# Kernel tuning notes

Hardware: AMD Instinct MI355X
Metric: run time of the kernel (lower is better)

## Reference

```python
import jax, jax.numpy as jnp
import numpy as np

B, T, I, H = 256, 512, 128, 256


def setup_inputs() -> dict:
    key = jax.random.key(0)
    ks = jax.random.split(key, 12)
    xav = lambda k, shape: jax.random.normal(k, shape, jnp.float32) * jnp.sqrt(2.0 / (shape[0] + shape[1]))
    return {
        'x': jax.random.normal(ks[0], (B, T, I), jnp.float32),
        'weight_xr': xav(ks[1], (H, I)), 'weight_hr': xav(ks[2], (H, H)), 'bias_r': jnp.zeros((H,), jnp.float32),
        'weight_xz': xav(ks[3], (H, I)), 'weight_hz': xav(ks[4], (H, H)), 'bias_z': jnp.zeros((H,), jnp.float32),
        'weight_x': xav(ks[5], (H, I)), 'weight_h': xav(ks[6], (H, H)), 'bias': jnp.zeros((H,), jnp.float32),
        'w1': xav(ks[7], (64, H)), 'b1': jnp.zeros((64,), jnp.float32),
        'w2': xav(ks[8], (10, 64)), 'b2': jnp.zeros((10,), jnp.float32),
    }


def _gru_final(x, weight_xr, weight_hr, bias_r, weight_xz, weight_hz, bias_z,
               weight_x, weight_h, bias):
    # Precompute input projections for all timesteps: [B,T,H] each
    xr = jnp.einsum('bti,hi->bth', x, weight_xr) + bias_r
    xz = jnp.einsum('bti,hi->bth', x, weight_xz) + bias_z
    xn = jnp.einsum('bti,hi->bth', x, weight_x) + bias

    def step(h, inp):
        xr_t, xz_t, xn_t = inp  # each [B,H]
        r = jax.nn.sigmoid(xr_t + h @ weight_hr.T)
        z = jax.nn.sigmoid(xz_t + h @ weight_hz.T)
        ht = jnp.tanh(xn_t + (r * h) @ weight_h.T)
        h_new = z * h + (1.0 - z) * ht
        return h_new, None

    h0 = jnp.zeros((x.shape[0], weight_hr.shape[0]), x.dtype)
    # scan over time: inputs [T,B,H]
    h_final, _ = jax.lax.scan(step, h0, (xr.transpose(1, 0, 2), xz.transpose(1, 0, 2), xn.transpose(1, 0, 2)))
    return h_final


def reference(x, weight_xr, weight_hr, bias_r, weight_xz, weight_hz, bias_z,
              weight_x, weight_h, bias, w1, b1, w2, b2):
    h = _gru_final(x, weight_xr, weight_hr, bias_r, weight_xz, weight_hz, bias_z,
                   weight_x, weight_h, bias)
    h = jax.nn.sigmoid(h)
    h = jax.nn.sigmoid(h @ w1.T + b1)
    return jax.nn.softmax(h @ w2.T + b2, axis=1)
```

## Files before the change

kernel.cpp:

```cpp
#include <hip/hip_runtime.h>


typedef _Float16 half8 __attribute__((ext_vector_type(8)));
typedef float    f32x4 __attribute__((ext_vector_type(4)));

#define BARRIER() asm volatile("s_waitcnt lgkmcnt(0)\n\ts_barrier" ::: "memory")

__device__ __forceinline__ unsigned short f2s(float f) {
    _Float16 h = (_Float16)f; unsigned short s; __builtin_memcpy(&s, &h, 2); return s;
}
__device__ __forceinline__ float s2f(unsigned short s) {
    _Float16 h; __builtin_memcpy(&h, &s, 2); return (float)h;
}
__device__ __forceinline__ float fast_sigmoid(float x) {
    return __builtin_amdgcn_rcpf(1.0f + __builtin_amdgcn_exp2f(-1.4426950408889634f * x));
}
__device__ __forceinline__ float fast_tanh(float x) {
    return 1.0f - 2.0f * __builtin_amdgcn_rcpf(1.0f + __builtin_amdgcn_exp2f(2.885390081777927f * x));
}
__device__ __forceinline__ unsigned int pk2(float lo, float hi) {
    return (unsigned int)f2s(lo) | ((unsigned int)f2s(hi) << 16);
}
union H8U4 { half8 h; uint4 u; };
__device__ __forceinline__ half8 ldg_h8(const unsigned short* p) {
    H8U4 t; t.u = *reinterpret_cast<const uint4*>(p); return t.h;
}
__device__ __forceinline__ half8 pack8(float4 a, float4 b) {
    half8 r;
    r[0] = (_Float16)a.x; r[1] = (_Float16)a.y; r[2] = (_Float16)a.z; r[3] = (_Float16)a.w;
    r[4] = (_Float16)b.x; r[5] = (_Float16)b.y; r[6] = (_Float16)b.z; r[7] = (_Float16)b.w;
    return r;
}

__global__ void pack_w_kernel(const float* __restrict__ whr, const float* __restrict__ whz,
                              const float* __restrict__ wh,  const float* __restrict__ wxr,
                              const float* __restrict__ wxz, const float* __restrict__ wxn,
                              unsigned short* __restrict__ Wall) {
    const int i = blockIdx.x * 256 + threadIdx.x;
    float v;
    if (i < 196608) {
        const int m = i >> 16;
        const int r = i & 65535;
        v = (m == 0 ? whr : (m == 1 ? whz : wh))[r];
    } else {
        const int ii = i - 196608;
        const int m = ii >> 15;
        const int r = ii & 32767;
        v = (m == 0 ? wxr : (m == 1 ? wxz : wxn))[r];
    }
    Wall[i] = f2s(v);
}

__global__ __launch_bounds__(256) void proj_kernel(
    const float* __restrict__ x, const unsigned short* __restrict__ Wxp,
    const float* __restrict__ br, const float* __restrict__ bz, const float* __restrict__ bn,
    unsigned short* __restrict__ P, int t0) {
    const int tid = threadIdx.x;
    const int wv  = tid >> 6;
    const int lane = tid & 63;
    const int l15 = lane & 15;
    const int lq  = lane >> 4;
    const int tl = blockIdx.x >> 4;
    const int btile = blockIdx.x & 15;
    const int t = t0 + tl;
    const int b0 = btile * 16;

    half8 xf[4];
#pragma unroll
    for (int kt = 0; kt < 4; ++kt) {
        const float* xp = x + (size_t)(b0 + l15) * 65536 + t * 128 + kt * 32 + 8 * lq;
        float4 f0 = *reinterpret_cast<const float4*>(xp);
        float4 f1 = *reinterpret_cast<const float4*>(xp + 4);
        xf[kt] = pack8(f0, f1);
    }
    const float* bptr[3] = {br, bz, bn};
    unsigned short* Pb = P + (size_t)tl * 196608 + btile * 12288;
#pragma unroll
    for (int g = 0; g < 3; ++g) {
#pragma unroll
        for (int ntl = 0; ntl < 4; ++ntl) {
            const int nt = wv * 4 + ntl;
            const int n0 = nt * 16;
            f32x4 acc = {0.f, 0.f, 0.f, 0.f};
#pragma unroll
            for (int kt = 0; kt < 4; ++kt) {
                half8 wf = ldg_h8(Wxp + g * 32768 + (n0 + l15) * 128 + kt * 32 + 8 * lq);
                acc = __builtin_amdgcn_mfma_f32_16x16x32_f16(wf, xf[kt], acc, 0, 0, 0);
            }
            float4 bv = *reinterpret_cast<const float4*>(bptr[g] + n0 + 4 * lq);
            uint2 o;
            o.x = pk2(acc[0] + bv.x, acc[1] + bv.y);
            o.y = pk2(acc[2] + bv.z, acc[3] + bv.w);
            *reinterpret_cast<uint2*>(Pb + nt * 768 + g * 256 + lane * 4) = o;
        }
    }
}

__global__ __launch_bounds__(512, 1) void rec_kernel(
    const unsigned short* __restrict__ Wp, const unsigned short* __restrict__ P,
    float* __restrict__ h_state, int t0, int Tc) {
    const int tid = threadIdx.x;
    const int w = tid >> 6;
    const int lane = tid & 63;
    const int l15 = lane & 15;
    const int lq = lane >> 4;
    const int btile = blockIdx.x;
    const int b0 = btile * 16;

    __shared__ __align__(16) unsigned short hl[8192];

    half8 wr[8][2], wz[8][2], wn[8][2];
#pragma unroll
    for (int kt = 0; kt < 8; ++kt) {
#pragma unroll
        for (int nt = 0; nt < 2; ++nt) {
            const int row = w * 32 + nt * 16 + l15;
            const int co = kt * 32 + 8 * lq;
            wr[kt][nt] = ldg_h8(Wp + row * 256 + co);
            wz[kt][nt] = ldg_h8(Wp + 65536 + row * 256 + co);
            wn[kt][nt] = ldg_h8(Wp + 131072 + row * 256 + co);
        }
    }

    const int b7 = l15 & 7;
    int rdaddr[8];
#pragma unroll
    for (int kt = 0; kt < 8; ++kt)
        rdaddr[kt] = l15 * 512 + (((4 * kt + lq) ^ b7) << 4);
    int waddr[2];
#pragma unroll
    for (int nt = 0; nt < 2; ++nt) {
        const int c = 4 * w + 2 * nt + (lq >> 1);
        waddr[nt] = l15 * 512 + ((c ^ b7) << 4) + 8 * (lq & 1);
    }

    float hreg[2][4];
    if (t0 == 0) {
#pragma unroll
        for (int nt = 0; nt < 2; ++nt)
#pragma unroll
            for (int j = 0; j < 4; ++j) hreg[nt][j] = 0.f;
    } else {
#pragma unroll
        for (int nt = 0; nt < 2; ++nt) {
            float4 v = *reinterpret_cast<const float4*>(
                h_state + (b0 + l15) * 256 + w * 32 + nt * 16 + 4 * lq);
            hreg[nt][0] = v.x; hreg[nt][1] = v.y; hreg[nt][2] = v.z; hreg[nt][3] = v.w;
        }
    }
#pragma unroll
    for (int nt = 0; nt < 2; ++nt) {
        uint2 o;
        o.x = pk2(hreg[nt][0], hreg[nt][1]);
        o.y = pk2(hreg[nt][2], hreg[nt][3]);
        *reinterpret_cast<uint2*>(reinterpret_cast<char*>(hl) + waddr[nt]) = o;
    }
    BARRIER();

    const unsigned short* Pw = P + btile * 12288 + (2 * w) * 768 + lane * 4;
    uint2 cp[3][2], np[3][2];
#pragma unroll
    for (int g = 0; g < 3; ++g)
#pragma unroll
        for (int nt = 0; nt < 2; ++nt)
            cp[g][nt] = *reinterpret_cast<const uint2*>(Pw + nt * 768 + g * 256);

    for (int tl = 0; tl < Tc; ++tl) {
        const unsigned short* Pn = Pw + (size_t)((tl + 1 < Tc) ? tl + 1 : tl) * 196608;
#pragma unroll
        for (int g = 0; g < 3; ++g)
#pragma unroll
            for (int nt = 0; nt < 2; ++nt)
                np[g][nt] = *reinterpret_cast<const uint2*>(Pn + nt * 768 + g * 256);

        f32x4 aR[2], aZ[2];
#pragma unroll
        for (int nt = 0; nt < 2; ++nt) {
            aR[nt] = (f32x4){ s2f((unsigned short)cp[0][nt].x), s2f((unsigned short)(cp[0][nt].x >> 16)),
                              s2f((unsigned short)cp[0][nt].y), s2f((unsigned short)(cp[0][nt].y >> 16)) };
            aZ[nt] = (f32x4){ s2f((unsigned short)cp[1][nt].x), s2f((unsigned short)(cp[1][nt].x >> 16)),
                              s2f((unsigned short)cp[1][nt].y), s2f((unsigned short)(cp[1][nt].y >> 16)) };
        }
#pragma unroll
        for (int kt = 0; kt < 8; ++kt) {
            half8 hf = *reinterpret_cast<const half8*>(reinterpret_cast<const char*>(hl) + rdaddr[kt]);
            aR[0] = __builtin_amdgcn_mfma_f32_16x16x32_f16(wr[kt][0], hf, aR[0], 0, 0, 0);
            aZ[0] = __builtin_amdgcn_mfma_f32_16x16x32_f16(wz[kt][0], hf, aZ[0], 0, 0, 0);
            aR[1] = __builtin_amdgcn_mfma_f32_16x16x32_f16(wr[kt][1], hf, aR[1], 0, 0, 0);
            aZ[1] = __builtin_amdgcn_mfma_f32_16x16x32_f16(wz[kt][1], hf, aZ[1], 0, 0, 0);
        }
        float zv[2][4];
#pragma unroll
        for (int nt = 0; nt < 2; ++nt) {
            float r0 = fast_sigmoid(aR[nt][0]);
            float r1 = fast_sigmoid(aR[nt][1]);
            float r2 = fast_sigmoid(aR[nt][2]);
            float r3 = fast_sigmoid(aR[nt][3]);
            zv[nt][0] = fast_sigmoid(aZ[nt][0]);
            zv[nt][1] = fast_sigmoid(aZ[nt][1]);
            zv[nt][2] = fast_sigmoid(aZ[nt][2]);
            zv[nt][3] = fast_sigmoid(aZ[nt][3]);
            uint2 o;
            o.x = pk2(r0 * hreg[nt][0], r1 * hreg[nt][1]);
            o.y = pk2(r2 * hreg[nt][2], r3 * hreg[nt][3]);
            *reinterpret_cast<uint2*>(reinterpret_cast<char*>(hl) + 8192 + waddr[nt]) = o;
        }
        BARRIER();

        f32x4 aN[2];
#pragma unroll
        for (int nt = 0; nt < 2; ++nt) {
            aN[nt] = (f32x4){ s2f((unsigned short)cp[2][nt].x), s2f((unsigned short)(cp[2][nt].x >> 16)),
                              s2f((unsigned short)cp[2][nt].y), s2f((unsigned short)(cp[2][nt].y >> 16)) };
        }
#pragma unroll
        for (int kt = 0; kt < 8; ++kt) {
            half8 rf = *reinterpret_cast<const half8*>(reinterpret_cast<const char*>(hl) + 8192 + rdaddr[kt]);
            aN[0] = __builtin_amdgcn_mfma_f32_16x16x32_f16(wn[kt][0], rf, aN[0], 0, 0, 0);
            aN[1] = __builtin_amdgcn_mfma_f32_16x16x32_f16(wn[kt][1], rf, aN[1], 0, 0, 0);
        }
#pragma unroll
        for (int nt = 0; nt < 2; ++nt) {
#pragma unroll
            for (int j = 0; j < 4; ++j) {
                const float ht = fast_tanh(aN[nt][j]);
                hreg[nt][j] = ht + zv[nt][j] * (hreg[nt][j] - ht);
            }
            uint2 o;
            o.x = pk2(hreg[nt][0], hreg[nt][1]);
            o.y = pk2(hreg[nt][2], hreg[nt][3]);
            *reinterpret_cast<uint2*>(reinterpret_cast<char*>(hl) + waddr[nt]) = o;
        }
        BARRIER();

#pragma unroll
        for (int g = 0; g < 3; ++g)
#pragma unroll
            for (int nt = 0; nt < 2; ++nt)
                cp[g][nt] = np[g][nt];
    }

#pragma unroll
    for (int nt = 0; nt < 2; ++nt) {
        float4 st;
        st.x = hreg[nt][0]; st.y = hreg[nt][1]; st.z = hreg[nt][2]; st.w = hreg[nt][3];
        *reinterpret_cast<float4*>(h_state + (b0 + l15) * 256 + w * 32 + nt * 16 + 4 * lq) = st;
    }
}

__global__ __launch_bounds__(64) void head_kernel(
    const float* __restrict__ h_state, const float* __restrict__ w1, const float* __restrict__ b1,
    const float* __restrict__ w2, const float* __restrict__ b2, float* __restrict__ out) {
    const int row = blockIdx.x;
    const int lane = threadIdx.x;
    __shared__ float hs[256];
    __shared__ float h2[64];
    __shared__ float lg[10];
    float4 v = *reinterpret_cast<const float4*>(h_state + row * 256 + lane * 4);
    hs[lane * 4 + 0] = fast_sigmoid(v.x);
    hs[lane * 4 + 1] = fast_sigmoid(v.y);
    hs[lane * 4 + 2] = fast_sigmoid(v.z);
    hs[lane * 4 + 3] = fast_sigmoid(v.w);
    __syncthreads();
    float acc = b1[lane];
#pragma unroll 4
    for (int k = 0; k < 256; k += 4) {
        float4 wv = *reinterpret_cast<const float4*>(w1 + lane * 256 + k);
        acc += hs[k] * wv.x + hs[k + 1] * wv.y + hs[k + 2] * wv.z + hs[k + 3] * wv.w;
    }
    h2[lane] = fast_sigmoid(acc);
    __syncthreads();
    if (lane < 10) {
        float a2 = b2[lane];
        for (int k = 0; k < 64; ++k) a2 += h2[k] * w2[lane * 64 + k];
        lg[lane] = a2;
    }
    __syncthreads();
    if (lane < 10) {
        float m = lg[0];
#pragma unroll
        for (int k = 1; k < 10; ++k) m = fmaxf(m, lg[k]);
        float s = 0.f;
#pragma unroll
        for (int k = 0; k < 10; ++k) s += __expf(lg[k] - m);
        out[row * 10 + lane] = __expf(lg[lane] - m) / s;
    }
}

extern "C" void kernel_launch(void* const* d_in, const int* in_sizes, int n_in,
                              void* d_out, int out_size, void* d_ws, size_t ws_size,
                              hipStream_t stream) {
    const float* x   = (const float*)d_in[0];
    const float* wxr = (const float*)d_in[1];
    const float* whr = (const float*)d_in[2];
    const float* br  = (const float*)d_in[3];
    const float* wxz = (const float*)d_in[4];
    const float* whz = (const float*)d_in[5];
    const float* bz  = (const float*)d_in[6];
    const float* wxn = (const float*)d_in[7];
    const float* wh  = (const float*)d_in[8];
    const float* bn  = (const float*)d_in[9];
    const float* w1  = (const float*)d_in[10];
    const float* b1  = (const float*)d_in[11];
    const float* w2  = (const float*)d_in[12];
    const float* b2  = (const float*)d_in[13];
    float* out = (float*)d_out;

    char* ws = (char*)d_ws;
    unsigned short* Wp  = (unsigned short*)ws;
    unsigned short* Wxp = (unsigned short*)(ws + 393216);
    float* h_state = (float*)(ws + 589824);
    unsigned short* P = (unsigned short*)(ws + 851968);
    const size_t avail = (ws_size > 851968) ? ws_size - 851968 : 0;
    int Tc = 512;
    while (Tc > 1 && (size_t)Tc * 393216 > avail) Tc >>= 1;

    pack_w_kernel<<<dim3(1152), 256, 0, stream>>>(whr, whz, wh, wxr, wxz, wxn, Wp);
    for (int t0 = 0; t0 < 512; t0 += Tc) {
        proj_kernel<<<dim3(Tc * 16), 256, 0, stream>>>(x, Wxp, br, bz, bn, P, t0);
        rec_kernel<<<dim3(16), 512, 0, stream>>>(Wp, P, h_state, t0, Tc);
    }
    head_kernel<<<dim3(256), 64, 0, stream>>>(h_state, w1, b1, w2, b2, out);
}
```

Measured before the change: 1.096 ms.

## Move z-gate MFMAs after barrier to shorten critical path; ping-pong prefetch buffers

The z-gate matmul moves out of the first phase so only the r-gate MFMAs sit before the first barrier. The z-gate and candidate MFMAs now run together after that barrier, which shortens the serial chain to the r*h write. All h and r*h fragments are loaded from LDS up front, and MFMA regions are wrapped in s_setprio. The loop is unrolled by two with swapped prefetch buffers to avoid register copies, which raises register pressure by keeping hf live across the barrier.

```diff
diff --git a/kernel.cpp b/kernel.cpp
--- a/kernel.cpp
+++ b/kernel.cpp
@@ -20,6 +20,10 @@
 }
 __device__ __forceinline__ unsigned int pk2(float lo, float hi) {
     return (unsigned int)f2s(lo) | ((unsigned int)f2s(hi) << 16);
+}
+__device__ __forceinline__ f32x4 up4(uint2 u) {
+    return (f32x4){ s2f((unsigned short)u.x), s2f((unsigned short)(u.x >> 16)),
+                    s2f((unsigned short)u.y), s2f((unsigned short)(u.y >> 16)) };
 }
 union H8U4 { half8 h; uint4 u; };
 __device__ __forceinline__ half8 ldg_h8(const unsigned short* p) {
@@ -108,6 +112,7 @@
     const int b0 = btile * 16;
 
     __shared__ __align__(16) unsigned short hl[8192];
+    char* lds = reinterpret_cast<char*>(hl);
 
     half8 wr[8][2], wz[8][2], wn[8][2];
 #pragma unroll
@@ -153,91 +158,102 @@
         uint2 o;
         o.x = pk2(hreg[nt][0], hreg[nt][1]);
         o.y = pk2(hreg[nt][2], hreg[nt][3]);
-        *reinterpret_cast<uint2*>(reinterpret_cast<char*>(hl) + waddr[nt]) = o;
+        *reinterpret_cast<uint2*>(lds + waddr[nt]) = o;
     }
     BARRIER();
 
     const unsigned short* Pw = P + btile * 12288 + (2 * w) * 768 + lane * 4;
-    uint2 cp[3][2], np[3][2];
+    uint2 cpA[3][2], cpB[3][2];
 #pragma unroll
     for (int g = 0; g < 3; ++g)
 #pragma unroll
         for (int nt = 0; nt < 2; ++nt)
-            cp[g][nt] = *reinterpret_cast<const uint2*>(Pw + nt * 768 + g * 256);
-
-    for (int tl = 0; tl < Tc; ++tl) {
-        const unsigned short* Pn = Pw + (size_t)((tl + 1 < Tc) ? tl + 1 : tl) * 196608;
+            cpA[g][nt] = *reinterpret_cast<const uint2*>(Pw + nt * 768 + g * 256);
+
+    auto STEP = [&](uint2 (&cp)[3][2], uint2 (&np)[3][2], const unsigned short* Pn) {
 #pragma unroll
         for (int g = 0; g < 3; ++g)
 #pragma unroll
             for (int nt = 0; nt < 2; ++nt)
                 np[g][nt] = *reinterpret_cast<const uint2*>(Pn + nt * 768 + g * 256);
 
-        f32x4 aR[2], aZ[2];
+        half8 hf[8];
+#pragma unroll
+        for (int kt = 0; kt < 8; ++kt)
+            hf[kt] = *reinterpret_cast<const half8*>(lds + rdaddr[kt]);
+        f32x4 aR[2];
+        aR[0] = up4(cp[0][0]);
+        aR[1] = up4(cp[0][1]);
+        __builtin_amdgcn_s_setprio(1);
+#pragma unroll
+        for (int kt = 0; kt < 8; ++kt) {
+            aR[0] = __builtin_amdgcn_mfma_f32_16x16x32_f16(wr[kt][0], hf[kt], aR[0], 0, 0, 0);
+            aR[1] = __builtin_amdgcn_mfma_f32_16x16x32_f16(wr[kt][1], hf[kt], aR[1], 0, 0, 0);
+        }
+        __builtin_amdgcn_s_setprio(0);
 #pragma unroll
         for (int nt = 0; nt < 2; ++nt) {
-            aR[nt] = (f32x4){ s2f((unsigned short)cp[0][nt].x), s2f((unsigned short)(cp[0][nt].x >> 16)),
-                              s2f((unsigned short)cp[0][nt].y), s2f((unsigned short)(cp[0][nt].y >> 16)) };
-            aZ[nt] = (f32x4){ s2f((unsigned short)cp[1][nt].x), s2f((unsigned short)(cp[1][nt].x >> 16)),
-                              s2f((unsigned short)cp[1][nt].y), s2f((unsigned short)(cp[1][nt].y >> 16)) };
-        }
-#pragma unroll
-        for (int kt = 0; kt < 8; ++kt) {
-            half8 hf = *reinterpret_cast<const half8*>(reinterpret_cast<const char*>(hl) + rdaddr[kt]);
-            aR[0] = __builtin_amdgcn_mfma_f32_16x16x32_f16(wr[kt][0], hf, aR[0], 0, 0, 0);
-            aZ[0] = __builtin_amdgcn_mfma_f32_16x16x32_f16(wz[kt][0], hf, aZ[0], 0, 0, 0);
-            aR[1] = __builtin_amdgcn_mfma_f32_16x16x32_f16(wr[kt][1], hf, aR[1], 0, 0, 0);
-            aZ[1] = __builtin_amdgcn_mfma_f32_16x16x32_f16(wz[kt][1], hf, aZ[1], 0, 0, 0);
-        }
-        float zv[2][4];
-#pragma unroll
-        for (int nt = 0; nt < 2; ++nt) {
-            float r0 = fast_sigmoid(aR[nt][0]);
-            float r1 = fast_sigmoid(aR[nt][1]);
-            float r2 = fast_sigmoid(aR[nt][2]);
-            float r3 = fast_sigmoid(aR[nt][3]);
-            zv[nt][0] = fast_sigmoid(aZ[nt][0]);
-            zv[nt][1] = fast_sigmoid(aZ[nt][1]);
-            zv[nt][2] = fast_sigmoid(aZ[nt][2]);
-            zv[nt][3] = fast_sigmoid(aZ[nt][3]);
+            const float r0 = fast_sigmoid(aR[nt][0]);
+            const float r1 = fast_sigmoid(aR[nt][1]);
+            const float r2 = fast_sigmoid(aR[nt][2]);
+            const float r3 = fast_sigmoid(aR[nt][3]);
             uint2 o;
             o.x = pk2(r0 * hreg[nt][0], r1 * hreg[nt][1]);
             o.y = pk2(r2 * hreg[nt][2], r3 * hreg[nt][3]);
-            *reinterpret_cast<uint2*>(reinterpret_cast<char*>(hl) + 8192 + waddr[nt]) = o;
+            *reinterpret_cast<uint2*>(lds + 8192 + waddr[nt]) = o;
         }
         BARRIER();
 
-        f32x4 aN[2];
+        half8 rf[8];
+#pragma unroll
+        for (int kt = 0; kt < 8; ++kt)
+            rf[kt] = *reinterpret_cast<const half8*>(lds + 8192 + rdaddr[kt]);
+        f32x4 aZ[2], aN[2];
+        aZ[0] = up4(cp[1][0]);
+        aZ[1] = up4(cp[1][1]);
+        aN[0] = up4(cp[2][0]);
+        aN[1] = up4(cp[2][1]);
+        __builtin_amdgcn_s_setprio(1);
+#pragma unroll
+        for (int kt = 0; kt < 8; ++kt) {
+            aZ[0] = __builtin_amdgcn_mfma_f32_16x16x32_f16(wz[kt][0], hf[kt], aZ[0], 0, 0, 0);
+            aZ[1] = __builtin_amdgcn_mfma_f32_16x16x32_f16(wz[kt][1], hf[kt], aZ[1], 0, 0, 0);
+        }
+#pragma unroll
+        for (int kt = 0; kt < 8; ++kt) {
+            aN[0] = __builtin_amdgcn_mfma_f32_16x16x32_f16(wn[kt][0], rf[kt], aN[0], 0, 0, 0);
+            aN[1] = __builtin_amdgcn_mfma_f32_16x16x32_f16(wn[kt][1], rf[kt], aN[1], 0, 0, 0);
+        }
+        __builtin_amdgcn_s_setprio(0);
 #pragma unroll
         for (int nt = 0; nt < 2; ++nt) {
-            aN[nt] = (f32x4){ s2f((unsigned short)cp[2][nt].x), s2f((unsigned short)(cp[2][nt].x >> 16)),
-                              s2f((unsigned short)cp[2][nt].y), s2f((unsigned short)(cp[2][nt].y >> 16)) };
-        }
-#pragma unroll
-        for (int kt = 0; kt < 8; ++kt) {
-            half8 rf = *reinterpret_cast<const half8*>(reinterpret_cast<const char*>(hl) + 8192 + rdaddr[kt]);
-            aN[0] = __builtin_amdgcn_mfma_f32_16x16x32_f16(wn[kt][0], rf, aN[0], 0, 0, 0);
-            aN[1] = __builtin_amdgcn_mfma_f32_16x16x32_f16(wn[kt][1], rf, aN[1], 0, 0, 0);
-        }
-#pragma unroll
-        for (int nt = 0; nt < 2; ++nt) {
-#pragma unroll
-            for (int j = 0; j < 4; ++j) {
-                const float ht = fast_tanh(aN[nt][j]);
-                hreg[nt][j] = ht + zv[nt][j] * (hreg[nt][j] - ht);
-            }
+            const float z0 = fast_sigmoid(aZ[nt][0]);
+            const float z1 = fast_sigmoid(aZ[nt][1]);
+            const float z2 = fast_sigmoid(aZ[nt][2]);
+            const float z3 = fast_sigmoid(aZ[nt][3]);
+            const float t0_ = fast_tanh(aN[nt][0]);
+            const float t1_ = fast_tanh(aN[nt][1]);
+            const float t2_ = fast_tanh(aN[nt][2]);
+            const float t3_ = fast_tanh(aN[nt][3]);
+            hreg[nt][0] = t0_ + z0 * (hreg[nt][0] - t0_);
+            hreg[nt][1] = t1_ + z1 * (hreg[nt][1] - t1_);
+            hreg[nt][2] = t2_ + z2 * (hreg[nt][2] - t2_);
+            hreg[nt][3] = t3_ + z3 * (hreg[nt][3] - t3_);
             uint2 o;
             o.x = pk2(hreg[nt][0], hreg[nt][1]);
             o.y = pk2(hreg[nt][2], hreg[nt][3]);
-            *reinterpret_cast<uint2*>(reinterpret_cast<char*>(hl) + waddr[nt]) = o;
+            *reinterpret_cast<uint2*>(lds + waddr[nt]) = o;
         }
         BARRIER();
-
-#pragma unroll
-        for (int g = 0; g < 3; ++g)
-#pragma unroll
-            for (int nt = 0; nt < 2; ++nt)
-                cp[g][nt] = np[g][nt];
+    };
+
+    for (int tl = 0; tl < Tc; tl += 2) {
+        const unsigned short* Pn1 = Pw + (size_t)((tl + 1 < Tc) ? tl + 1 : Tc - 1) * 196608;
+        STEP(cpA, cpB, Pn1);
+        if (tl + 1 < Tc) {
+            const unsigned short* Pn2 = Pw + (size_t)((tl + 2 < Tc) ? tl + 2 : Tc - 1) * 196608;
+            STEP(cpB, cpA, Pn2);
+        }
     }
 
 #pragma unroll
```

After: 2.790 ms. 2.55x slower.
